# Kernel tuning notes

Measured on AMD Instinct MI355X. Metric: run time of the kernel, lower is better.

Reference implementation:

```python
import jax, jax.numpy as jnp
import numpy as np

DIM = 192; EXP = 2; QKB = 4
INNER = EXP * DIM          # 384
NH = INNER // QKB          # 96 heads
DH = QKB                   # 4 dims per head
Hs, Ws = 24, 24; S = Hs * Ws; B = 1; K = 3
EPS = 1e-6


def setup_inputs() -> dict:
    key = jax.random.key(0)
    ks = jax.random.split(key, 16)
    sm_up = (2.0 / (5.0 * DIM)) ** 0.5
    sm_dn = (2.0 / (5.0 * INNER)) ** 0.5
    def n(k, shape, s):
        return jax.random.normal(k, shape, jnp.float32) * s
    return {
        "x": jax.random.normal(ks[0], (B, S, DIM), jnp.float32),
        "d": jax.random.normal(ks[1], (B, S, DIM), jnp.float32),
        "ln_w": jnp.ones((DIM,), jnp.float32),
        "ln_b": jnp.zeros((DIM,), jnp.float32),
        "up_w": n(ks[2], (2 * INNER, DIM), sm_up),
        "up_b": jnp.zeros((2 * INNER,), jnp.float32),
        "dup_w": n(ks[3], (INNER, DIM), sm_up),
        "dup_b": jnp.zeros((INNER,), jnp.float32),
        "q_w": n(ks[4], (NH, DH, DH), sm_up), "q_b": jnp.zeros((INNER,), jnp.float32),
        "k_w": n(ks[5], (NH, DH, DH), sm_up), "k_b": jnp.zeros((INNER,), jnp.float32),
        "v_w": n(ks[6], (NH, DH, DH), sm_up), "v_b": jnp.zeros((INNER,), jnp.float32),
        "conv_w": n(ks[7], (INNER, K, K), 0.1), "conv_b": jnp.zeros((INNER,), jnp.float32),
        "ig_w": n(ks[8], (NH, 3 * INNER), 0.01),
        "ig_b": jax.random.normal(ks[9], (NH,), jnp.float32) * 0.1 - 3.0,
        "fg_w": jnp.zeros((NH, 3 * INNER), jnp.float32),
        "fg_b": jnp.linspace(3.0, 6.0, NH, dtype=jnp.float32),
        "onorm_w": jnp.ones((INNER,), jnp.float32),
        "skip": jnp.ones((INNER,), jnp.float32),
        "down_w": n(ks[10], (DIM, INNER), sm_dn),
        "down_b": jnp.zeros((DIM,), jnp.float32),
    }


def _headwise(x, w, b):
    # LinearHeadwiseExpand: block-diagonal linear, per-head DHxDH matrix
    Bx, Sx, _ = x.shape
    y = jnp.einsum('bsni,noi->bsno', x.reshape(Bx, Sx, NH, DH), w)
    return y.reshape(Bx, Sx, INNER) + b


def _mlstm(q, k, v, ig, fg, onorm_w):
    # parallel_stabilized_simple: q,k,v [B,NH,S,DH]; ig,fg [B,NH,S]
    Sq = q.shape[2]
    log_f = jax.nn.log_sigmoid(fg)                    # [B,NH,S]
    lfc = jnp.cumsum(log_f, axis=-1)                  # cumulative log forget
    logfm = lfc[..., :, None] - lfc[..., None, :]     # [B,NH,S,S]
    mask = jnp.tril(jnp.ones((Sq, Sq), dtype=bool))
    logD = jnp.where(mask, logfm + ig[..., None, :], -jnp.inf)
    maxD = jnp.max(logD, axis=-1, keepdims=True)      # [B,NH,S,1] stabilizer
    Dm = jnp.exp(logD - maxD)
    C = jnp.einsum('bnsd,bntd->bnst', q, k / (DH ** 0.5)) * Dm
    norm = jnp.maximum(jnp.abs(C.sum(-1, keepdims=True)), jnp.exp(-maxD))
    h = jnp.einsum('bnst,bntd->bnsd', C / (norm + EPS), v)
    # MultiHeadLayerNorm (group norm over DH per head, weight only)
    mu = h.mean(-1, keepdims=True)
    var = h.var(-1, keepdims=True)
    return (h - mu) / jnp.sqrt(var + 1e-5) * onorm_w.reshape(NH, DH)[None, :, None, :]


def _forward(x, d, ln_w, ln_b, up_w, up_b, dup_w, dup_b, q_w, q_b, k_w, k_b,
             v_w, v_b, conv_w, conv_b, ig_w, ig_b, fg_w, fg_b, onorm_w, skip,
             down_w, down_b):
    Bx, Sx, _ = x.shape
    # pre-norm LayerNorm
    mu = x.mean(-1, keepdims=True)
    var = x.var(-1, keepdims=True)
    xn = (x - mu) / jnp.sqrt(var + 1e-5) * ln_w + ln_b
    x_inner = xn @ up_w.T + up_b                      # [B,S,2*INNER]
    x_mlstm, z = jnp.split(x_inner, 2, axis=-1)
    d_mlstm = d @ dup_w.T + dup_b                     # dead code in original forward
    # depthwise 3x3 conv over the HxW token grid (SequenceConv2d, groups=INNER)
    kern = jnp.transpose(conv_w, (1, 2, 0))[:, :, None, :]   # HWIO
    xc = jax.lax.conv_general_dilated(
        x_mlstm.reshape(Bx, Hs, Ws, INNER), kern, (1, 1), 'SAME',
        dimension_numbers=('NHWC', 'HWIO', 'NHWC'),
        feature_group_count=INNER) + conv_b
    xa = jax.nn.silu(xc.reshape(Bx, Sx, INNER))
    q = _headwise(xa, q_w, q_b)
    k = _headwise(xa, k_w, k_b)
    v = _headwise(x_mlstm, v_w, v_b)
    gin = jnp.concatenate([q, k, v], axis=-1)         # [B,S,3*INNER]
    ig = (gin @ ig_w.T + ig_b).transpose(0, 2, 1)     # [B,NH,S]
    fg = (gin @ fg_w.T + fg_b).transpose(0, 2, 1)
    to_h = lambda t: t.reshape(Bx, Sx, NH, DH).transpose(0, 2, 1, 3)
    h = _mlstm(to_h(q), to_h(k), to_h(v), ig, fg, onorm_w)   # [B,NH,S,DH]
    h = h.transpose(0, 2, 1, 3).reshape(Bx, Sx, INNER)
    h = (h + skip * xa) * jax.nn.silu(z)
    return h @ down_w.T + down_b


def reference(x, d, ln_w, ln_b, up_w, up_b, dup_w, dup_b, q_w, q_b, k_w, k_b,
              v_w, v_b, conv_w, conv_b, ig_w, ig_b, fg_w, fg_b, onorm_w, skip,
              down_w, down_b):
    return _forward(x, d, ln_w, ln_b, up_w, up_b, dup_w, dup_b, q_w, q_b,
                    k_w, k_b, v_w, v_b, conv_w, conv_b, ig_w, ig_b, fg_w,
                    fg_b, onorm_w, skip, down_w, down_b)
```

## Files before the change

### kernel.cpp

```cpp
#include <hip/hip_runtime.h>
#include <math.h>

#define SEQ 576
#define DIM 192
#define INNER 384
#define NHEAD 96
#define HS 24
#define WSZ 24
#define GIN 1152
#define GKS 4

#define UPA 68
#define UPB 36
__global__ __launch_bounds__(256) void k_up(const float* __restrict__ x,
    const float* __restrict__ lnw, const float* __restrict__ lnb,
    const float* __restrict__ w, const float* __restrict__ b,
    float* __restrict__ out) {
  int m0 = blockIdx.x * 64, n0 = blockIdx.y * 32;
  __shared__ float As[DIM * UPA];
  __shared__ float Bs[DIM * UPB];
  __shared__ float mu[64], inv[64], ps[192];
  int t = threadIdx.x;
  for (int idx = t; idx < 64 * 48; idx += 256) {
    int r = idx / 48, k4 = idx % 48;
    float4 v = *(const float4*)&x[(m0 + r) * DIM + 4 * k4];
    As[(4 * k4 + 0) * UPA + r] = v.x;
    As[(4 * k4 + 1) * UPA + r] = v.y;
    As[(4 * k4 + 2) * UPA + r] = v.z;
    As[(4 * k4 + 3) * UPA + r] = v.w;
  }
  for (int idx = t; idx < 32 * 48; idx += 256) {
    int r = idx / 48, k4 = idx % 48;
    float4 v = *(const float4*)&w[(n0 + r) * DIM + 4 * k4];
    Bs[(4 * k4 + 0) * UPB + r] = v.x;
    Bs[(4 * k4 + 1) * UPB + r] = v.y;
    Bs[(4 * k4 + 2) * UPB + r] = v.z;
    Bs[(4 * k4 + 3) * UPB + r] = v.w;
  }
  __syncthreads();
  if (t < 192) {
    int r = t % 64, ph = t / 64;
    float s_ = 0.f;
    #pragma unroll 8
    for (int k = ph * 64; k < ph * 64 + 64; ++k) s_ += As[k * UPA + r];
    ps[t] = s_;
  }
  __syncthreads();
  if (t < 64) mu[t] = (ps[t] + ps[64 + t] + ps[128 + t]) * (1.0f / DIM);
  __syncthreads();
  if (t < 192) {
    int r = t % 64, ph = t / 64;
    float m_ = mu[r], s_ = 0.f;
    #pragma unroll 8
    for (int k = ph * 64; k < ph * 64 + 64; ++k) {
      float d = As[k * UPA + r] - m_; s_ += d * d;
    }
    ps[t] = s_;
  }
  __syncthreads();
  if (t < 64) inv[t] = rsqrtf((ps[t] + ps[64 + t] + ps[128 + t]) * (1.0f / DIM) + 1e-5f);
  __syncthreads();
  for (int idx = t; idx < 64 * DIM; idx += 256) {
    int k = idx / 64, r = idx % 64;
    As[k * UPA + r] = (As[k * UPA + r] - mu[r]) * inv[r] * lnw[k] + lnb[k];
  }
  __syncthreads();
  int gm = t >> 4, gn = t & 15;
  float acc[4][2];
  #pragma unroll
  for (int i = 0; i < 4; ++i)
    #pragma unroll
    for (int j = 0; j < 2; ++j) acc[i][j] = b[n0 + 2 * gn + j];
  #pragma unroll 4
  for (int kk = 0; kk < DIM; ++kk) {
    float4 a = *(const float4*)&As[kk * UPA + 4 * gm];
    float2 bv = *(const float2*)&Bs[kk * UPB + 2 * gn];
    acc[0][0] += a.x * bv.x; acc[0][1] += a.x * bv.y;
    acc[1][0] += a.y * bv.x; acc[1][1] += a.y * bv.y;
    acc[2][0] += a.z * bv.x; acc[2][1] += a.z * bv.y;
    acc[3][0] += a.w * bv.x; acc[3][1] += a.w * bv.y;
  }
  #pragma unroll
  for (int i = 0; i < 4; ++i)
    *(float2*)&out[(m0 + 4 * gm + i) * (2 * INNER) + n0 + 2 * gn] =
        make_float2(acc[i][0], acc[i][1]);
}

__global__ __launch_bounds__(384) void k_cqkv(const float* __restrict__ xin,
    const float* __restrict__ cw, const float* __restrict__ cb,
    const float* __restrict__ qw, const float* __restrict__ qb,
    const float* __restrict__ kw, const float* __restrict__ kb,
    const float* __restrict__ vw, const float* __restrict__ vb,
    float* __restrict__ xa, float* __restrict__ ginT) {
  int s = blockIdx.x, t = threadIdx.x;
  int h = s / WSZ, wc = s % WSZ;
  __shared__ float xat[INNER], xmt[INNER];
  float acc = cb[t];
  #pragma unroll
  for (int kh = 0; kh < 3; ++kh) {
    int hh = h + kh - 1;
    if (hh < 0 || hh >= HS) continue;
    #pragma unroll
    for (int kw2 = 0; kw2 < 3; ++kw2) {
      int ww = wc + kw2 - 1;
      if (ww < 0 || ww >= WSZ) continue;
      acc += xin[(hh * WSZ + ww) * (2 * INNER) + t] * cw[t * 9 + kh * 3 + kw2];
    }
  }
  float sil = acc / (1.0f + __expf(-acc));
  xat[t] = sil;
  xa[s * INNER + t] = sil;
  xmt[t] = xin[s * (2 * INNER) + t];
  __syncthreads();
  int n = t >> 2, o = t & 3;
  const float* xah = xat + n * 4;
  const float* xmh = xmt + n * 4;
  float q = qb[t], k = kb[t], v = vb[t];
  #pragma unroll
  for (int i = 0; i < 4; ++i) {
    float xq = xah[i], xm = xmh[i];
    q += xq * qw[n * 16 + o * 4 + i];
    k += xq * kw[n * 16 + o * 4 + i];
    v += xm * vw[n * 16 + o * 4 + i];
  }
  ginT[t * SEQ + s]               = q;
  ginT[(INNER + t) * SEQ + s]     = k;
  ginT[(2 * INNER + t) * SEQ + s] = v;
}

#define GBK 288
#define WP 36
__global__ __launch_bounds__(256) void k_gates(const float* __restrict__ ginT,
    const float* __restrict__ igw, const float* __restrict__ fgw,
    float* __restrict__ pig, float* __restrict__ pfg) {
  int bx = blockIdx.x, s0 = blockIdx.y * 64, ks = blockIdx.z;
  int k0 = ks * GBK;
  bool isig = bx < 3;
  int m0 = (isig ? bx : bx - 3) * 32;
  const float* wb = (isig ? igw : fgw) + m0 * GIN;
  __shared__ float Ws[GBK * WP];
  __shared__ float Gs[GBK * 64];
  int t = threadIdx.x;
  for (int idx = t; idx < 32 * 72; idx += 256) {
    int r = idx / 72, k4 = idx % 72;
    float4 v = *(const float4*)&wb[r * GIN + k0 + 4 * k4];
    Ws[(4 * k4 + 0) * WP + r] = v.x;
    Ws[(4 * k4 + 1) * WP + r] = v.y;
    Ws[(4 * k4 + 2) * WP + r] = v.z;
    Ws[(4 * k4 + 3) * WP + r] = v.w;
  }
  for (int idx = t; idx < GBK * 16; idx += 256) {
    int kk = idx / 16, s4 = idx % 16;
    *(float4*)&Gs[kk * 64 + 4 * s4] =
        *(const float4*)&ginT[(k0 + kk) * SEQ + s0 + 4 * s4];
  }
  __syncthreads();
  int gm = t >> 4, gn = t & 15;
  float acc[2][4] = {{0.f,0.f,0.f,0.f},{0.f,0.f,0.f,0.f}};
  #pragma unroll 4
  for (int kk = 0; kk < GBK; ++kk) {
    float2 wv = *(const float2*)&Ws[kk * WP + 2 * gm];
    float4 gv = *(const float4*)&Gs[kk * 64 + 4 * gn];
    acc[0][0] += wv.x * gv.x; acc[0][1] += wv.x * gv.y;
    acc[0][2] += wv.x * gv.z; acc[0][3] += wv.x * gv.w;
    acc[1][0] += wv.y * gv.x; acc[1][1] += wv.y * gv.y;
    acc[1][2] += wv.y * gv.z; acc[1][3] += wv.y * gv.w;
  }
  float* dstp = (isig ? pig : pfg) + ks * NHEAD * SEQ;
  #pragma unroll
  for (int i = 0; i < 2; ++i) {
    int mm = m0 + 2 * gm + i;
    *(float4*)&dstp[mm * SEQ + s0 + 4 * gn] =
        make_float4(acc[i][0], acc[i][1], acc[i][2], acc[i][3]);
  }
}

__global__ __launch_bounds__(576) void k_mlstm(const float* __restrict__ ginT,
    const float* __restrict__ pig, const float* __restrict__ pfg,
    const float* __restrict__ igb, const float* __restrict__ fgb,
    const float* __restrict__ onw, float* __restrict__ hout) {
  int n = blockIdx.x, hh = blockIdx.y, t = threadIdx.x;
  int cnt2 = 288 * (hh + 1);
  __shared__ float ksm[SEQ * 4], vsm[SEQ * 4], esm[SEQ];
  __shared__ float bufA[SEQ], bufB[SEQ], bufC[SEQ];
  const int H4 = NHEAD * SEQ;
  float ai = 0.f;
  if (t < cnt2) {
    float a0 = ginT[(INNER + n * 4 + 0) * SEQ + t] * 0.5f;
    float a1 = ginT[(INNER + n * 4 + 1) * SEQ + t] * 0.5f;
    float a2 = ginT[(INNER + n * 4 + 2) * SEQ + t] * 0.5f;
    float a3 = ginT[(INNER + n * 4 + 3) * SEQ + t] * 0.5f;
    *(float4*)&ksm[t * 4] = make_float4(a0, a1, a2, a3);
    float b0 = ginT[(2 * INNER + n * 4 + 0) * SEQ + t];
    float b1 = ginT[(2 * INNER + n * 4 + 1) * SEQ + t];
    float b2 = ginT[(2 * INNER + n * 4 + 2) * SEQ + t];
    float b3 = ginT[(2 * INNER + n * 4 + 3) * SEQ + t];
    *(float4*)&vsm[t * 4] = make_float4(b0, b1, b2, b3);
    int off = n * SEQ + t;
    ai = igb[n] + pig[off] + pig[off + H4] + pig[off + 2 * H4] + pig[off + 3 * H4];
    float af = fgb[n] + pfg[off] + pfg[off + H4] + pfg[off + 2 * H4] + pfg[off + 3 * H4];
    float lf = (af >= 0.f) ? -log1pf(expf(-af)) : (af - log1pf(expf(af)));
    bufA[t] = lf;
  }
  __syncthreads();
  float* src = bufA; float* dst = bufB;
  for (int o2 = 1; o2 < cnt2; o2 <<= 1) {
    if (t < cnt2) {
      float v = src[t];
      if (t >= o2) v += src[t - o2];
      dst[t] = v;
    }
    __syncthreads();
    float* tmp = src; src = dst; dst = tmp;
  }
  if (t < cnt2) {
    float e = ai - src[t];
    esm[t] = e;
    dst[t] = e;
  }
  __syncthreads();
  float* srcM = dst; float* dstM = bufC;
  for (int o2 = 1; o2 < cnt2; o2 <<= 1) {
    if (t < cnt2) {
      float v = srcM[t];
      if (t >= o2) v = fmaxf(v, srcM[t - o2]);
      dstM[t] = v;
    }
    __syncthreads();
    float* tmp = srcM; srcM = dstM; dstM = tmp;
  }
  int r = (t < 288) ? t : t - 288;
  int half = (t >= 288) ? 1 : 0;
  int s = 288 * hh + r;
  float pm = srcM[s];
  float mxv = src[s] + pm;
  float q0 = ginT[(n * 4 + 0) * SEQ + s];
  float q1 = ginT[(n * 4 + 1) * SEQ + s];
  float q2 = ginT[(n * 4 + 2) * SEQ + s];
  float q3 = ginT[(n * 4 + 3) * SEQ + s];
  int N = s + 1, nA = (N + 1) >> 1;
  int lo = half ? nA : 0, hi = half ? N : nA;
  float csum = 0.f, h0 = 0.f, h1 = 0.f, h2 = 0.f, h3 = 0.f;
  for (int tt = lo; tt < hi; ++tt) {
    float d = __expf(esm[tt] - pm);
    float c = (q0 * ksm[tt*4] + q1 * ksm[tt*4+1] + q2 * ksm[tt*4+2] + q3 * ksm[tt*4+3]) * d;
    csum += c;
    h0 += c * vsm[tt*4]; h1 += c * vsm[tt*4+1]; h2 += c * vsm[tt*4+2]; h3 += c * vsm[tt*4+3];
  }
  __syncthreads();
  if (half) {
    ksm[r * 5 + 0] = csum; ksm[r * 5 + 1] = h0; ksm[r * 5 + 2] = h1;
    ksm[r * 5 + 3] = h2;   ksm[r * 5 + 4] = h3;
  }
  __syncthreads();
  if (!half) {
    csum += ksm[r * 5 + 0];
    h0 += ksm[r * 5 + 1]; h1 += ksm[r * 5 + 2];
    h2 += ksm[r * 5 + 3]; h3 += ksm[r * 5 + 4];
    float norm = fmaxf(fabsf(csum), __expf(-mxv)) + 1e-6f;
    float rr = 1.0f / norm;
    h0 *= rr; h1 *= rr; h2 *= rr; h3 *= rr;
    float mu = (h0 + h1 + h2 + h3) * 0.25f;
    float d0 = h0 - mu, d1 = h1 - mu, d2 = h2 - mu, d3 = h3 - mu;
    float var = (d0 * d0 + d1 * d1 + d2 * d2 + d3 * d3) * 0.25f;
    float inv = rsqrtf(var + 1e-5f);
    *(float4*)&hout[s * INNER + n * 4] = make_float4(
        d0 * inv * onw[n * 4 + 0], d1 * inv * onw[n * 4 + 1],
        d2 * inv * onw[n * 4 + 2], d3 * inv * onw[n * 4 + 3]);
  }
}

#define DNA 20
#define DNB 36
__global__ __launch_bounds__(128) void k_down(const float* __restrict__ hmat,
    const float* __restrict__ xa, const float* __restrict__ xin,
    const float* __restrict__ skip, const float* __restrict__ dw,
    const float* __restrict__ db, float* __restrict__ out) {
  int m0 = blockIdx.x * 16, n0 = blockIdx.y * 32;
  __shared__ float As[INNER * DNA];
  __shared__ float Bs[INNER * DNB];
  int t = threadIdx.x;
  for (int idx = t; idx < 16 * 96; idx += 128) {
    int r = idx / 96, k4 = idx % 96;
    int s = m0 + r;
    float4 zv = *(const float4*)&xin[s * (2 * INNER) + INNER + 4 * k4];
    float4 hm = *(const float4*)&hmat[s * INNER + 4 * k4];
    float4 xv = *(const float4*)&xa[s * INNER + 4 * k4];
    float4 sk = *(const float4*)&skip[4 * k4];
    float z, sil;
    z = zv.x; sil = z / (1.0f + __expf(-z));
    As[(4 * k4 + 0) * DNA + r] = (hm.x + sk.x * xv.x) * sil;
    z = zv.y; sil = z / (1.0f + __expf(-z));
    As[(4 * k4 + 1) * DNA + r] = (hm.y + sk.y * xv.y) * sil;
    z = zv.z; sil = z / (1.0f + __expf(-z));
    As[(4 * k4 + 2) * DNA + r] = (hm.z + sk.z * xv.z) * sil;
    z = zv.w; sil = z / (1.0f + __expf(-z));
    As[(4 * k4 + 3) * DNA + r] = (hm.w + sk.w * xv.w) * sil;
  }
  for (int idx = t; idx < 32 * 96; idx += 128) {
    int r = idx / 96, k4 = idx % 96;
    float4 v = *(const float4*)&dw[(n0 + r) * INNER + 4 * k4];
    Bs[(4 * k4 + 0) * DNB + r] = v.x;
    Bs[(4 * k4 + 1) * DNB + r] = v.y;
    Bs[(4 * k4 + 2) * DNB + r] = v.z;
    Bs[(4 * k4 + 3) * DNB + r] = v.w;
  }
  __syncthreads();
  int gm = t >> 4, gn = t & 15;
  float acc[2][2];
  #pragma unroll
  for (int i = 0; i < 2; ++i)
    #pragma unroll
    for (int j = 0; j < 2; ++j) acc[i][j] = db[n0 + 2 * gn + j];
  #pragma unroll 4
  for (int kk = 0; kk < INNER; ++kk) {
    float2 a = *(const float2*)&As[kk * DNA + 2 * gm];
    float2 bv = *(const float2*)&Bs[kk * DNB + 2 * gn];
    acc[0][0] += a.x * bv.x; acc[0][1] += a.x * bv.y;
    acc[1][0] += a.y * bv.x; acc[1][1] += a.y * bv.y;
  }
  #pragma unroll
  for (int i = 0; i < 2; ++i)
    *(float2*)&out[(m0 + 2 * gm + i) * DIM + n0 + 2 * gn] =
        make_float2(acc[i][0], acc[i][1]);
}

extern "C" void kernel_launch(void* const* d_in, const int* in_sizes, int n_in,
                              void* d_out, int out_size, void* d_ws, size_t ws_size,
                              hipStream_t stream) {
  const float* x      = (const float*)d_in[0];
  const float* ln_w   = (const float*)d_in[2];
  const float* ln_b   = (const float*)d_in[3];
  const float* up_w   = (const float*)d_in[4];
  const float* up_b   = (const float*)d_in[5];
  const float* q_w    = (const float*)d_in[8];
  const float* q_b    = (const float*)d_in[9];
  const float* k_w    = (const float*)d_in[10];
  const float* k_b    = (const float*)d_in[11];
  const float* v_w    = (const float*)d_in[12];
  const float* v_b    = (const float*)d_in[13];
  const float* conv_w = (const float*)d_in[14];
  const float* conv_b = (const float*)d_in[15];
  const float* ig_w   = (const float*)d_in[16];
  const float* ig_b   = (const float*)d_in[17];
  const float* fg_w   = (const float*)d_in[18];
  const float* fg_b   = (const float*)d_in[19];
  const float* onorm_w= (const float*)d_in[20];
  const float* skip   = (const float*)d_in[21];
  const float* down_w = (const float*)d_in[22];
  const float* down_b = (const float*)d_in[23];
  float* out = (float*)d_out;

  float* ws     = (float*)d_ws;
  float* xinner = ws;
  float* xa     = xinner + SEQ * 2 * INNER;
  float* ginT   = xa + SEQ * INNER;
  float* pig    = ginT + GIN * SEQ;
  float* pfg    = pig + GKS * NHEAD * SEQ;
  float* hbuf   = pfg + GKS * NHEAD * SEQ;

  k_up   <<<dim3(9, 24), 256, 0, stream>>>(x, ln_w, ln_b, up_w, up_b, xinner);
  k_cqkv <<<SEQ, 384, 0, stream>>>(xinner, conv_w, conv_b,
                                   q_w, q_b, k_w, k_b, v_w, v_b, xa, ginT);
  k_gates<<<dim3(6, 9, GKS), 256, 0, stream>>>(ginT, ig_w, fg_w, pig, pfg);
  k_mlstm<<<dim3(NHEAD, 2), 576, 0, stream>>>(ginT, pig, pfg, ig_b, fg_b, onorm_w, hbuf);
  k_down <<<dim3(36, 6), 128, 0, stream>>>(hbuf, xa, xinner, skip, down_w, down_b, out);
}
```

Before: 102.2 us.

## Use XOR-swizzled shared tiles and larger per-thread register tiles in GEMM kernels

The up-projection, gate and down-projection GEMM kernels replace padded shared-memory layouts with XOR-swizzled unpadded layouts. They also halve the threads per block so each thread computes a 4x4 (or 2x4) output tile with float4 shared loads. The down kernel keeps the A operand row-major with padding instead of transposing it. This aims to raise FLOPs per shared-memory load and avoid bank conflicts. The cost is fewer threads for the load and LayerNorm phases and fewer wavefronts per block on small grids.

```diff
diff --git a/kernel.cpp b/kernel.cpp
--- a/kernel.cpp
+++ b/kernel.cpp
@@ -10,80 +10,86 @@
 #define GIN 1152
 #define GKS 4
 
-#define UPA 68
-#define UPB 36
-__global__ __launch_bounds__(256) void k_up(const float* __restrict__ x,
+__global__ __launch_bounds__(128) void k_up(const float* __restrict__ x,
     const float* __restrict__ lnw, const float* __restrict__ lnb,
     const float* __restrict__ w, const float* __restrict__ b,
     float* __restrict__ out) {
   int m0 = blockIdx.x * 64, n0 = blockIdx.y * 32;
-  __shared__ float As[DIM * UPA];
-  __shared__ float Bs[DIM * UPB];
-  __shared__ float mu[64], inv[64], ps[192];
+  __shared__ float As[DIM * 64];
+  __shared__ float Bs[DIM * 32];
+  __shared__ float mu[64], inv[64], ps[128];
   int t = threadIdx.x;
-  for (int idx = t; idx < 64 * 48; idx += 256) {
+  for (int idx = t; idx < 64 * 48; idx += 128) {
     int r = idx / 48, k4 = idx % 48;
     float4 v = *(const float4*)&x[(m0 + r) * DIM + 4 * k4];
-    As[(4 * k4 + 0) * UPA + r] = v.x;
-    As[(4 * k4 + 1) * UPA + r] = v.y;
-    As[(4 * k4 + 2) * UPA + r] = v.z;
-    As[(4 * k4 + 3) * UPA + r] = v.w;
-  }
-  for (int idx = t; idx < 32 * 48; idx += 256) {
+    int rw = r ^ (4 * (k4 & 15));
+    As[(4 * k4 + 0) * 64 + rw] = v.x;
+    As[(4 * k4 + 1) * 64 + rw] = v.y;
+    As[(4 * k4 + 2) * 64 + rw] = v.z;
+    As[(4 * k4 + 3) * 64 + rw] = v.w;
+  }
+  for (int idx = t; idx < 32 * 48; idx += 128) {
     int r = idx / 48, k4 = idx % 48;
     float4 v = *(const float4*)&w[(n0 + r) * DIM + 4 * k4];
-    Bs[(4 * k4 + 0) * UPB + r] = v.x;
-    Bs[(4 * k4 + 1) * UPB + r] = v.y;
-    Bs[(4 * k4 + 2) * UPB + r] = v.z;
-    Bs[(4 * k4 + 3) * UPB + r] = v.w;
-  }
-  __syncthreads();
-  if (t < 192) {
-    int r = t % 64, ph = t / 64;
+    int rw = r ^ (4 * (k4 & 7));
+    Bs[(4 * k4 + 0) * 32 + rw] = v.x;
+    Bs[(4 * k4 + 1) * 32 + rw] = v.y;
+    Bs[(4 * k4 + 2) * 32 + rw] = v.z;
+    Bs[(4 * k4 + 3) * 32 + rw] = v.w;
+  }
+  __syncthreads();
+  {
+    int r = t & 63, ph = t >> 6;
     float s_ = 0.f;
     #pragma unroll 8
-    for (int k = ph * 64; k < ph * 64 + 64; ++k) s_ += As[k * UPA + r];
+    for (int k = ph * 96; k < ph * 96 + 96; ++k)
+      s_ += As[k * 64 + (r ^ (4 * ((k >> 2) & 15)))];
     ps[t] = s_;
   }
   __syncthreads();
-  if (t < 64) mu[t] = (ps[t] + ps[64 + t] + ps[128 + t]) * (1.0f / DIM);
-  __syncthreads();
-  if (t < 192) {
-    int r = t % 64, ph = t / 64;
+  if (t < 64) mu[t] = (ps[t] + ps[t + 64]) * (1.0f / DIM);
+  __syncthreads();
+  {
+    int r = t & 63, ph = t >> 6;
     float m_ = mu[r], s_ = 0.f;
     #pragma unroll 8
-    for (int k = ph * 64; k < ph * 64 + 64; ++k) {
-      float d = As[k * UPA + r] - m_; s_ += d * d;
+    for (int k = ph * 96; k < ph * 96 + 96; ++k) {
+      float d = As[k * 64 + (r ^ (4 * ((k >> 2) & 15)))] - m_;
+      s_ += d * d;
     }
     ps[t] = s_;
   }
   __syncthreads();
-  if (t < 64) inv[t] = rsqrtf((ps[t] + ps[64 + t] + ps[128 + t]) * (1.0f / DIM) + 1e-5f);
-  __syncthreads();
-  for (int idx = t; idx < 64 * DIM; idx += 256) {
-    int k = idx / 64, r = idx % 64;
-    As[k * UPA + r] = (As[k * UPA + r] - mu[r]) * inv[r] * lnw[k] + lnb[k];
-  }
-  __syncthreads();
-  int gm = t >> 4, gn = t & 15;
-  float acc[4][2];
+  if (t < 64) inv[t] = rsqrtf((ps[t] + ps[t + 64]) * (1.0f / DIM) + 1e-5f);
+  __syncthreads();
+  for (int idx = t; idx < 64 * DIM; idx += 128) {
+    int k = idx >> 6, r0 = idx & 63;
+    int m = r0 ^ (4 * ((k >> 2) & 15));
+    As[idx] = (As[idx] - mu[m]) * inv[m] * lnw[k] + lnb[k];
+  }
+  __syncthreads();
+  int gm = t >> 3, gn = t & 7;
+  float acc[4][4];
   #pragma unroll
   for (int i = 0; i < 4; ++i)
     #pragma unroll
-    for (int j = 0; j < 2; ++j) acc[i][j] = b[n0 + 2 * gn + j];
+    for (int j = 0; j < 4; ++j) acc[i][j] = b[n0 + 4 * gn + j];
   #pragma unroll 4
   for (int kk = 0; kk < DIM; ++kk) {
-    float4 a = *(const float4*)&As[kk * UPA + 4 * gm];
-    float2 bv = *(const float2*)&Bs[kk * UPB + 2 * gn];
-    acc[0][0] += a.x * bv.x; acc[0][1] += a.x * bv.y;
-    acc[1][0] += a.y * bv.x; acc[1][1] += a.y * bv.y;
-    acc[2][0] += a.z * bv.x; acc[2][1] += a.z * bv.y;
-    acc[3][0] += a.w * bv.x; acc[3][1] += a.w * bv.y;
+    int mk = (kk >> 2) & 15, nk = (kk >> 2) & 7;
+    float4 a = *(const float4*)&As[kk * 64 + 4 * (gm ^ mk)];
+    float4 bv = *(const float4*)&Bs[kk * 32 + 4 * (gn ^ nk)];
+    #pragma unroll
+    for (int i = 0; i < 4; ++i) {
+      float av = (i == 0) ? a.x : (i == 1) ? a.y : (i == 2) ? a.z : a.w;
+      acc[i][0] += av * bv.x; acc[i][1] += av * bv.y;
+      acc[i][2] += av * bv.z; acc[i][3] += av * bv.w;
+    }
   }
   #pragma unroll
   for (int i = 0; i < 4; ++i)
-    *(float2*)&out[(m0 + 4 * gm + i) * (2 * INNER) + n0 + 2 * gn] =
-        make_float2(acc[i][0], acc[i][1]);
+    *(float4*)&out[(m0 + 4 * gm + i) * (2 * INNER) + n0 + 4 * gn] =
+        make_float4(acc[i][0], acc[i][1], acc[i][2], acc[i][3]);
 }
 
 __global__ __launch_bounds__(384) void k_cqkv(const float* __restrict__ xin,
@@ -129,8 +135,7 @@
 }
 
 #define GBK 288
-#define WP 36
-__global__ __launch_bounds__(256) void k_gates(const float* __restrict__ ginT,
+__global__ __launch_bounds__(128) void k_gates(const float* __restrict__ ginT,
     const float* __restrict__ igw, const float* __restrict__ fgw,
     float* __restrict__ pig, float* __restrict__ pfg) {
   int bx = blockIdx.x, s0 = blockIdx.y * 64, ks = blockIdx.z;
@@ -138,38 +143,46 @@
   bool isig = bx < 3;
   int m0 = (isig ? bx : bx - 3) * 32;
   const float* wb = (isig ? igw : fgw) + m0 * GIN;
-  __shared__ float Ws[GBK * WP];
+  __shared__ float Ws[GBK * 32];
   __shared__ float Gs[GBK * 64];
   int t = threadIdx.x;
-  for (int idx = t; idx < 32 * 72; idx += 256) {
+  for (int idx = t; idx < 32 * 72; idx += 128) {
     int r = idx / 72, k4 = idx % 72;
     float4 v = *(const float4*)&wb[r * GIN + k0 + 4 * k4];
-    Ws[(4 * k4 + 0) * WP + r] = v.x;
-    Ws[(4 * k4 + 1) * WP + r] = v.y;
-    Ws[(4 * k4 + 2) * WP + r] = v.z;
-    Ws[(4 * k4 + 3) * WP + r] = v.w;
-  }
-  for (int idx = t; idx < GBK * 16; idx += 256) {
+    int rw = r ^ (4 * (k4 & 7));
+    Ws[(4 * k4 + 0) * 32 + rw] = v.x;
+    Ws[(4 * k4 + 1) * 32 + rw] = v.y;
+    Ws[(4 * k4 + 2) * 32 + rw] = v.z;
+    Ws[(4 * k4 + 3) * 32 + rw] = v.w;
+  }
+  for (int idx = t; idx < GBK * 16; idx += 128) {
     int kk = idx / 16, s4 = idx % 16;
     *(float4*)&Gs[kk * 64 + 4 * s4] =
         *(const float4*)&ginT[(k0 + kk) * SEQ + s0 + 4 * s4];
   }
   __syncthreads();
   int gm = t >> 4, gn = t & 15;
-  float acc[2][4] = {{0.f,0.f,0.f,0.f},{0.f,0.f,0.f,0.f}};
+  float acc[4][4];
+  #pragma unroll
+  for (int i = 0; i < 4; ++i)
+    #pragma unroll
+    for (int j = 0; j < 4; ++j) acc[i][j] = 0.f;
   #pragma unroll 4
   for (int kk = 0; kk < GBK; ++kk) {
-    float2 wv = *(const float2*)&Ws[kk * WP + 2 * gm];
+    int mk = (kk >> 2) & 7;
+    float4 wv = *(const float4*)&Ws[kk * 32 + 4 * (gm ^ mk)];
     float4 gv = *(const float4*)&Gs[kk * 64 + 4 * gn];
-    acc[0][0] += wv.x * gv.x; acc[0][1] += wv.x * gv.y;
-    acc[0][2] += wv.x * gv.z; acc[0][3] += wv.x * gv.w;
-    acc[1][0] += wv.y * gv.x; acc[1][1] += wv.y * gv.y;
-    acc[1][2] += wv.y * gv.z; acc[1][3] += wv.y * gv.w;
+    #pragma unroll
+    for (int i = 0; i < 4; ++i) {
+      float av = (i == 0) ? wv.x : (i == 1) ? wv.y : (i == 2) ? wv.z : wv.w;
+      acc[i][0] += av * gv.x; acc[i][1] += av * gv.y;
+      acc[i][2] += av * gv.z; acc[i][3] += av * gv.w;
+    }
   }
   float* dstp = (isig ? pig : pfg) + ks * NHEAD * SEQ;
   #pragma unroll
-  for (int i = 0; i < 2; ++i) {
-    int mm = m0 + 2 * gm + i;
+  for (int i = 0; i < 4; ++i) {
+    int mm = m0 + 4 * gm + i;
     *(float4*)&dstp[mm * SEQ + s0 + 4 * gn] =
         make_float4(acc[i][0], acc[i][1], acc[i][2], acc[i][3]);
   }
@@ -270,17 +283,16 @@
   }
 }
 
-#define DNA 20
-#define DNB 36
-__global__ __launch_bounds__(128) void k_down(const float* __restrict__ hmat,
+#define KPA 388
+__global__ __launch_bounds__(64) void k_down(const float* __restrict__ hmat,
     const float* __restrict__ xa, const float* __restrict__ xin,
     const float* __restrict__ skip, const float* __restrict__ dw,
     const float* __restrict__ db, float* __restrict__ out) {
   int m0 = blockIdx.x * 16, n0 = blockIdx.y * 32;
-  __shared__ float As[INNER * DNA];
-  __shared__ float Bs[INNER * DNB];
+  __shared__ float As[16 * KPA];
+  __shared__ float Bs[INNER * 32];
   int t = threadIdx.x;
-  for (int idx = t; idx < 16 * 96; idx += 128) {
+  for (int idx = t; idx < 16 * 96; idx += 64) {
     int r = idx / 96, k4 = idx % 96;
     int s = m0 + r;
     float4 zv = *(const float4*)&xin[s * (2 * INNER) + INNER + 4 * k4];
@@ -288,41 +300,44 @@
     float4 xv = *(const float4*)&xa[s * INNER + 4 * k4];
     float4 sk = *(const float4*)&skip[4 * k4];
     float z, sil;
-    z = zv.x; sil = z / (1.0f + __expf(-z));
-    As[(4 * k4 + 0) * DNA + r] = (hm.x + sk.x * xv.x) * sil;
-    z = zv.y; sil = z / (1.0f + __expf(-z));
-    As[(4 * k4 + 1) * DNA + r] = (hm.y + sk.y * xv.y) * sil;
-    z = zv.z; sil = z / (1.0f + __expf(-z));
-    As[(4 * k4 + 2) * DNA + r] = (hm.z + sk.z * xv.z) * sil;
-    z = zv.w; sil = z / (1.0f + __expf(-z));
-    As[(4 * k4 + 3) * DNA + r] = (hm.w + sk.w * xv.w) * sil;
-  }
-  for (int idx = t; idx < 32 * 96; idx += 128) {
+    float4 o;
+    z = zv.x; sil = z / (1.0f + __expf(-z)); o.x = (hm.x + sk.x * xv.x) * sil;
+    z = zv.y; sil = z / (1.0f + __expf(-z)); o.y = (hm.y + sk.y * xv.y) * sil;
+    z = zv.z; sil = z / (1.0f + __expf(-z)); o.z = (hm.z + sk.z * xv.z) * sil;
+    z = zv.w; sil = z / (1.0f + __expf(-z)); o.w = (hm.w + sk.w * xv.w) * sil;
+    *(float4*)&As[r * KPA + 4 * k4] = o;
+  }
+  for (int idx = t; idx < 32 * 96; idx += 64) {
     int r = idx / 96, k4 = idx % 96;
     float4 v = *(const float4*)&dw[(n0 + r) * INNER + 4 * k4];
-    Bs[(4 * k4 + 0) * DNB + r] = v.x;
-    Bs[(4 * k4 + 1) * DNB + r] = v.y;
-    Bs[(4 * k4 + 2) * DNB + r] = v.z;
-    Bs[(4 * k4 + 3) * DNB + r] = v.w;
-  }
-  __syncthreads();
-  int gm = t >> 4, gn = t & 15;
-  float acc[2][2];
+    int rw = r ^ (4 * (k4 & 7));
+    Bs[(4 * k4 + 0) * 32 + rw] = v.x;
+    Bs[(4 * k4 + 1) * 32 + rw] = v.y;
+    Bs[(4 * k4 + 2) * 32 + rw] = v.z;
+    Bs[(4 * k4 + 3) * 32 + rw] = v.w;
+  }
+  __syncthreads();
+  int gm = t >> 3, gn = t & 7;
+  float acc[2][4];
   #pragma unroll
   for (int i = 0; i < 2; ++i)
     #pragma unroll
-    for (int j = 0; j < 2; ++j) acc[i][j] = db[n0 + 2 * gn + j];
+    for (int j = 0; j < 4; ++j) acc[i][j] = db[n0 + 4 * gn + j];
   #pragma unroll 4
   for (int kk = 0; kk < INNER; ++kk) {
-    float2 a = *(const float2*)&As[kk * DNA + 2 * gm];
-    float2 bv = *(const float2*)&Bs[kk * DNB + 2 * gn];
-    acc[0][0] += a.x * bv.x; acc[0][1] += a.x * bv.y;
-    acc[1][0] += a.y * bv.x; acc[1][1] += a.y * bv.y;
+    int nk = (kk >> 2) & 7;
+    float a0 = As[(2 * gm) * KPA + kk];
+    float a1 = As[(2 * gm + 1) * KPA + kk];
+    float4 bv = *(const float4*)&Bs[kk * 32 + 4 * (gn ^ nk)];
+    acc[0][0] += a0 * bv.x; acc[0][1] += a0 * bv.y;
+    acc[0][2] += a0 * bv.z; acc[0][3] += a0 * bv.w;
+    acc[1][0] += a1 * bv.x; acc[1][1] += a1 * bv.y;
+    acc[1][2] += a1 * bv.z; acc[1][3] += a1 * bv.w;
   }
   #pragma unroll
   for (int i = 0; i < 2; ++i)
-    *(float2*)&out[(m0 + 2 * gm + i) * DIM + n0 + 2 * gn] =
-        make_float2(acc[i][0], acc[i][1]);
+    *(float4*)&out[(m0 + 2 * gm + i) * DIM + n0 + 4 * gn] =
+        make_float4(acc[i][0], acc[i][1], acc[i][2], acc[i][3]);
 }
 
 extern "C" void kernel_launch(void* const* d_in, const int* in_sizes, int n_in,
@@ -359,10 +374,10 @@
   float* pfg    = pig + GKS * NHEAD * SEQ;
   float* hbuf   = pfg + GKS * NHEAD * SEQ;
 
-  k_up   <<<dim3(9, 24), 256, 0, stream>>>(x, ln_w, ln_b, up_w, up_b, xinner);
+  k_up   <<<dim3(9, 24), 128, 0, stream>>>(x, ln_w, ln_b, up_w, up_b, xinner);
   k_cqkv <<<SEQ, 384, 0, stream>>>(xinner, conv_w, conv_b,
                                    q_w, q_b, k_w, k_b, v_w, v_b, xa, ginT);
-  k_gates<<<dim3(6, 9, GKS), 256, 0, stream>>>(ginT, ig_w, fg_w, pig, pfg);
+  k_gates<<<dim3(6, 9, GKS), 128, 0, stream>>>(ginT, ig_w, fg_w, pig, pfg);
   k_mlstm<<<dim3(NHEAD, 2), 576, 0, stream>>>(ginT, pig, pfg, ig_b, fg_b, onorm_w, hbuf);
-  k_down <<<dim3(36, 6), 128, 0, stream>>>(hbuf, xa, xinner, skip, down_w, down_b, out);
-}
+  k_down <<<dim3(36, 6), 64, 0, stream>>>(hbuf, xa, xinner, skip, down_w, down_b, out);
+}
```

Result: slower. 136.1 us (+33.1%).
